# Performance work log

Hardware: AMD Instinct MI355X
Metric: run time of the kernel (lower is better)

Reference implementation:

```python
import jax, jax.numpy as jnp
import numpy as np

L, B, T, C, H, V = 4, 4, 1024, 1024, 16, 32000
DH = C // H
FF = 4 * C
IGNORE = 5
EPS = 1e-5


def setup_inputs() -> dict:
    key = jax.random.key(0)
    ks = jax.random.split(key, 12)
    s = 0.02
    return {
        "idx": jax.random.randint(ks[0], (B, T), 0, V),
        "targets": jax.random.randint(ks[1], (B, T), 0, V),
        "tok_emb": jax.random.normal(ks[2], (V, C), jnp.float32) * s,
        "pos_emb": jax.random.normal(ks[3], (T, C), jnp.float32) * s,
        "Wq": jax.random.normal(ks[4], (L, C, C), jnp.float32) * s,
        "Wk": jax.random.normal(ks[5], (L, C, C), jnp.float32) * s,
        "Wv": jax.random.normal(ks[6], (L, C, C), jnp.float32) * s,
        "Wo": jax.random.normal(ks[7], (L, C, C), jnp.float32) * s,
        "bo": jnp.zeros((L, C), jnp.float32),
        "ln1_g": jnp.ones((L, C), jnp.float32),
        "ln1_b": jnp.zeros((L, C), jnp.float32),
        "ln2_g": jnp.ones((L, C), jnp.float32),
        "ln2_b": jnp.zeros((L, C), jnp.float32),
        "W1": jax.random.normal(ks[8], (L, C, FF), jnp.float32) * s,
        "b1": jnp.zeros((L, FF), jnp.float32),
        "W2": jax.random.normal(ks[9], (L, FF, C), jnp.float32) * s,
        "b2": jnp.zeros((L, C), jnp.float32),
        "lnf_g": jnp.ones((C,), jnp.float32),
        "lnf_b": jnp.zeros((C,), jnp.float32),
        "Whead": jax.random.normal(ks[10], (C, V), jnp.float32) * s,
        "bhead": jnp.zeros((V,), jnp.float32),
    }


def _layernorm(x, g, b):
    mu = jnp.mean(x, axis=-1, keepdims=True)
    var = jnp.var(x, axis=-1, keepdims=True)
    return (x - mu) * jax.lax.rsqrt(var + EPS) * g + b


def _gpt_forward(idx, targets, tok_emb, pos_emb, Wq, Wk, Wv, Wo, bo,
                 ln1_g, ln1_b, ln2_g, ln2_b, W1, b1, W2, b2,
                 lnf_g, lnf_b, Whead, bhead):
    x = tok_emb[idx] + pos_emb[None, :, :]  # [B,T,C]
    causal = jnp.tril(jnp.ones((T, T), bool))
    for i in range(L):
        h = _layernorm(x, ln1_g[i], ln1_b[i])
        q = (h @ Wq[i]).reshape(B, T, H, DH)
        k = (h @ Wk[i]).reshape(B, T, H, DH)
        v = (h @ Wv[i]).reshape(B, T, H, DH)
        wei = jnp.einsum("bqhd,bkhd->bhqk", q, k) * (DH ** -0.5)
        wei = jnp.where(causal[None, None], wei, -jnp.inf)
        wei = jax.nn.softmax(wei, axis=-1)
        att = jnp.einsum("bhqk,bkhd->bqhd", wei, v).reshape(B, T, C)
        x = x + att @ Wo[i] + bo[i]
        h = _layernorm(x, ln2_g[i], ln2_b[i])
        x = x + jax.nn.gelu(h @ W1[i] + b1[i], approximate=False) @ W2[i] + b2[i]
    x = _layernorm(x, lnf_g, lnf_b)
    logits = x @ Whead + bhead  # [B,T,V]
    # cross-entropy with ignore_index=5
    lg = logits.reshape(B * T, V)
    tg = targets.reshape(B * T)
    logp = jax.nn.log_softmax(lg, axis=-1)
    nll = -jnp.take_along_axis(logp, tg[:, None], axis=-1)[:, 0]
    valid = (tg != IGNORE).astype(lg.dtype)
    loss = jnp.sum(nll * valid) / jnp.maximum(jnp.sum(valid), 1.0)
    return logits, loss


def reference(idx, targets, tok_emb, pos_emb, Wq, Wk, Wv, Wo, bo,
              ln1_g, ln1_b, ln2_g, ln2_b, W1, b1, W2, b2,
              lnf_g, lnf_b, Whead, bhead):
    return _gpt_forward(idx, targets, tok_emb, pos_emb, Wq, Wk, Wv, Wo, bo,
                        ln1_g, ln1_b, ln2_g, ln2_b, W1, b1, W2, b2,
                        lnf_g, lnf_b, Whead, bhead)
```

## Files before the change

kernel.cpp:

```cpp
#include <hip/hip_runtime.h>
#include <cstdint>
#include <cstddef>

#define Lx 4
#define Bx 4
#define Tx 1024
#define Cx 1024
#define Hx 16
#define DHx 64
#define FFx 4096
#define Vx 32000
#define BTx 4096

typedef __attribute__((ext_vector_type(8))) __bf16 bf16x8;
typedef __attribute__((ext_vector_type(4))) float f32x4;
typedef __attribute__((ext_vector_type(8))) short short8;

__device__ __forceinline__ float bflo(unsigned u){ return __builtin_bit_cast(float, u << 16); }
__device__ __forceinline__ float bf2f(short s){ return bflo((unsigned)(unsigned short)s); }
__device__ __forceinline__ short f2bf(float f){
  unsigned u = __builtin_bit_cast(unsigned, f);
  u += 0x7fffu + ((u >> 16) & 1u);
  return (short)(u >> 16);
}

__device__ __forceinline__ void gload_lds16(const short* g, short* l){
  __builtin_amdgcn_global_load_lds(
      (const __attribute__((address_space(1))) unsigned int*)g,
      (__attribute__((address_space(3))) unsigned int*)l, 16, 0, 0);
}

__device__ __forceinline__ int xcd_swizzle(int orig, int nwg){
  const int q = nwg >> 3, r = nwg & 7;
  const int xcd = orig & 7, wg = orig >> 3;
  const int base = (xcd < r) ? xcd * (q + 1) : r * (q + 1) + (xcd - r) * q;
  return base + wg;
}

__global__ __launch_bounds__(256) void embed_kernel(
    const int* __restrict__ idx, const float* __restrict__ tok,
    const float* __restrict__ pos, float* __restrict__ x)
{
  const int bt = blockIdx.x;
  const int t  = bt & (Tx - 1);
  const int tid = threadIdx.x;
  const int tk = idx[bt];
  float4 a = *(const float4*)&tok[((size_t)tk << 10) + (tid << 2)];
  const float4 p = *(const float4*)&pos[((size_t)t << 10) + (tid << 2)];
  a.x += p.x; a.y += p.y; a.z += p.z; a.w += p.w;
  *(float4*)&x[((size_t)bt << 10) + (tid << 2)] = a;
}

__global__ __launch_bounds__(256) void ln_kernel(
    const float* __restrict__ x, const float* __restrict__ g,
    const float* __restrict__ b, short* __restrict__ out)
{
  const int row = blockIdx.x;
  const int tid = threadIdx.x;
  const float4 v = *(const float4*)&x[((size_t)row << 10) + (tid << 2)];
  float s  = v.x + v.y + v.z + v.w;
  float ss = v.x*v.x + v.y*v.y + v.z*v.z + v.w*v.w;
  #pragma unroll
  for (int off = 32; off >= 1; off >>= 1) {
    s  += __shfl_down(s, off);
    ss += __shfl_down(ss, off);
  }
  __shared__ float rs[4], rss[4];
  const int lane = tid & 63, w = tid >> 6;
  if (lane == 0) { rs[w] = s; rss[w] = ss; }
  __syncthreads();
  s  = rs[0] + rs[1] + rs[2] + rs[3];
  ss = rss[0] + rss[1] + rss[2] + rss[3];
  const float mu  = s * (1.0f / Cx);
  const float var = ss * (1.0f / Cx) - mu * mu;
  const float rstd = rsqrtf(var + 1e-5f);
  const float4 g4 = *(const float4*)&g[tid << 2];
  const float4 b4 = *(const float4*)&b[tid << 2];
  short4 o;
  o.x = f2bf((v.x - mu) * rstd * g4.x + b4.x);
  o.y = f2bf((v.y - mu) * rstd * g4.y + b4.y);
  o.z = f2bf((v.z - mu) * rstd * g4.z + b4.z);
  o.w = f2bf((v.w - mu) * rstd * g4.w + b4.w);
  *(short4*)&out[((size_t)row << 10) + (tid << 2)] = o;
}

__global__ __launch_bounds__(256) void wconv_kernel(
    const float* __restrict__ W, short* __restrict__ Wt, int K, int N)
{
  __shared__ float tile[32][33];
  const int n0 = blockIdx.x << 5, k0 = blockIdx.y << 5;
  const int tx = threadIdx.x & 31, ty = threadIdx.x >> 5;
  #pragma unroll
  for (int r = 0; r < 4; ++r)
    tile[ty + (r << 3)][tx] = __builtin_nontemporal_load(
        &W[(size_t)(k0 + ty + (r << 3)) * N + n0 + tx]);
  __syncthreads();
  #pragma unroll
  for (int r = 0; r < 4; ++r)
    Wt[(size_t)(n0 + ty + (r << 3)) * K + k0 + tx] = f2bf(tile[tx][ty + (r << 3)]);
}

__global__ __launch_bounds__(256) void wconv4_kernel(
    const float* __restrict__ Wq, const float* __restrict__ Wk,
    const float* __restrict__ Wv, const float* __restrict__ Wo,
    short* __restrict__ qkvT, short* __restrict__ woT)
{
  __shared__ float tile[32][33];
  const int z = blockIdx.z;
  const float* W = (z == 0) ? Wq : (z == 1) ? Wk : (z == 2) ? Wv : Wo;
  short* Wt = (z < 3) ? qkvT + (size_t)z * Cx * Cx : woT;
  const int n0 = blockIdx.x << 5, k0 = blockIdx.y << 5;
  const int tx = threadIdx.x & 31, ty = threadIdx.x >> 5;
  #pragma unroll
  for (int r = 0; r < 4; ++r)
    tile[ty + (r << 3)][tx] = __builtin_nontemporal_load(
        &W[(size_t)(k0 + ty + (r << 3)) * Cx + n0 + tx]);
  __syncthreads();
  #pragma unroll
  for (int r = 0; r < 4; ++r)
    Wt[(size_t)(n0 + ty + (r << 3)) * Cx + k0 + tx] = f2bf(tile[tx][ty + (r << 3)]);
}

template<int MODE>
__global__ __launch_bounds__(256) void gemm_kernel(
    const short* __restrict__ A, const short* __restrict__ Bt,
    const float* __restrict__ bias, const float* __restrict__ res,
    float* __restrict__ outF, short* __restrict__ outB, int N, int K)
{
  __shared__ __align__(16) short sA[128 * 32];
  __shared__ __align__(16) short sB[128 * 32];
  const int tid  = threadIdx.x;
  const int lane = tid & 63;
  const int wave = tid >> 6;
  const int bid  = xcd_swizzle((int)blockIdx.x, (int)gridDim.x);
  const int tm = (bid & 31) << 7;
  const int tn = (bid >> 5) << 7;
  const int wm = ((wave >> 1) & 1) << 6;
  const int wn = (wave & 1) << 6;

  f32x4 acc[4][4] = {};

  const int o1  = tid << 4;
  const int row = o1 >> 6;
  const int col = (o1 & 63) >> 1;
  const short* gA1 = A  + (size_t)(tm + row) * K + col;
  const short* gA2 = A  + (size_t)(tm + row + 64) * K + col;
  const short* gB1 = Bt + (size_t)(tn + row) * K + col;
  const short* gB2 = Bt + (size_t)(tn + row + 64) * K + col;
  short* lA1 = sA + (wave << 9);
  short* lA2 = sA + 2048 + (wave << 9);
  short* lB1 = sB + (wave << 9);
  short* lB2 = sB + 2048 + (wave << 9);

  for (int k0 = 0; k0 < K; k0 += 32) {
    gload_lds16(gA1 + k0, lA1);
    gload_lds16(gA2 + k0, lA2);
    gload_lds16(gB1 + k0, lB1);
    gload_lds16(gB2 + k0, lB2);
    __syncthreads();
    bf16x8 aF[4], bF[4];
    const int kb = (lane >> 4) << 3;
    const int rsel = lane & 15;
    #pragma unroll
    for (int m = 0; m < 4; ++m)
      aF[m] = *(const bf16x8*)&sA[(wm + m * 16 + rsel) * 32 + kb];
    #pragma unroll
    for (int n = 0; n < 4; ++n)
      bF[n] = *(const bf16x8*)&sB[(wn + n * 16 + rsel) * 32 + kb];
    #pragma unroll
    for (int m = 0; m < 4; ++m) {
      #pragma unroll
      for (int n = 0; n < 4; ++n)
        acc[m][n] = __builtin_amdgcn_mfma_f32_16x16x32_bf16(aF[m], bF[n], acc[m][n], 0, 0, 0);
    }
    __syncthreads();
  }

  const int r0 = (lane >> 4) << 2;
  const int c0 = lane & 15;
  #pragma unroll
  for (int m = 0; m < 4; ++m) {
    #pragma unroll
    for (int n = 0; n < 4; ++n) {
      #pragma unroll
      for (int r = 0; r < 4; ++r) {
        const int grow = tm + wm + m * 16 + r0 + r;
        const int gcol = tn + wn + n * 16 + c0;
        const float v = acc[m][n][r];
        if constexpr (MODE == 0) {
          const int which = gcol >> 10;
          const int cc = gcol & 1023;
          const int b = grow >> 10, t = grow & 1023;
          const int hh = cc >> 6, d = cc & 63;
          outB[(size_t)which * (BTx * Cx) +
               ((size_t)((((b << 4) + hh) << 10) + t) << 6) + d] = f2bf(v);
        } else {
          const size_t o = (size_t)grow * N + gcol;
          outF[o] = res[o] + v + bias[gcol];
        }
      }
    }
  }
}

#define GBAR() do { __builtin_amdgcn_sched_barrier(0); __builtin_amdgcn_s_barrier(); __builtin_amdgcn_sched_barrier(0); } while(0)
#define VM4 asm volatile("s_waitcnt vmcnt(4)" ::: "memory");
#define VM0 asm volatile("s_waitcnt vmcnt(0)" ::: "memory");
#define NOWAIT

#define PHASE(qq, dd, STAGES, ENDW) do { \
  aF[0][0] = RD_A(dd, qq, 0, 0); aF[0][1] = RD_A(dd, qq, 0, 1); \
  aF[1][0] = RD_A(dd, qq, 1, 0); aF[1][1] = RD_A(dd, qq, 1, 1); \
  STAGES \
  GBAR(); \
  asm volatile("s_waitcnt lgkmcnt(0)" ::: "memory"); \
  __builtin_amdgcn_sched_barrier(0); \
  __builtin_amdgcn_s_setprio(1); \
  _Pragma("unroll") \
  for (int ks = 0; ks < 2; ++ks) { \
    _Pragma("unroll") \
    for (int mf = 0; mf < 2; ++mf) { \
      _Pragma("unroll") \
      for (int nf = 0; nf < 4; ++nf) \
        acc[((qq) << 1) + mf][nf] = __builtin_amdgcn_mfma_f32_16x16x32_bf16( \
            aF[mf][ks], bF[nf][ks], acc[((qq) << 1) + mf][nf], 0, 0, 0); \
    } \
  } \
  __builtin_amdgcn_s_setprio(0); \
  ENDW \
  GBAR(); \
} while (0)

#define BLOAD(dd) do { \
  _Pragma("unroll") \
  for (int nf = 0; nf < 4; ++nf) { bF[nf][0] = RD_B(dd, nf, 0); bF[nf][1] = RD_B(dd, nf, 1); } \
} while (0)

#define FINISH(qq) do { \
  _Pragma("unroll") \
  for (int m8 = ((qq) << 1); m8 < ((qq) << 1) + 2; ++m8) { \
    _Pragma("unroll") \
    for (int nf = 0; nf < 4; ++nf) { \
      _Pragma("unroll") \
      for (int r = 0; r < 4; ++r) { \
        const int grow = tm + (wm << 7) + (m8 << 4) + (g4 << 2) + r; \
        const int gcol = tn + (wn << 6) + (nf << 4) + r15; \
        if constexpr (MODE == 3) { \
          acc[m8][nf][r] += bb4[nf]; \
          outF[(size_t)grow * N + gcol] = acc[m8][nf][r]; \
        } else { \
          const float t2 = acc[m8][nf][r] + bb4[nf]; \
          const float gl = 0.5f * t2 * (1.0f + erff(t2 * 0.7071067811865475f)); \
          outB[(size_t)grow * N + gcol] = f2bf(gl); \
        } \
      } \
    } \
  } \
} while (0)

template<int MODE>
__global__ __launch_bounds__(512, 2) void gemm256_kernel(
    const short* __restrict__ A, const short* __restrict__ Bt,
    const float* __restrict__ bias, float* __restrict__ outF,
    short* __restrict__ outB, float* __restrict__ cep, int N, int K)
{
  __shared__ __align__(16) char lds[131072];
  const int tid  = threadIdx.x;
  const int lane = tid & 63;
  const int wid  = tid >> 6;
  const int wm   = wid >> 2;
  const int wn   = wid & 3;
  const int r15  = lane & 15;
  const int g4   = lane >> 4;
  const int bid  = xcd_swizzle((int)blockIdx.x, (int)gridDim.x);
  const int tm   = (bid & 15) << 8;
  const int tn   = (bid >> 4) << 8;
  const int NT   = K >> 6;
  const int NI   = NT >> 1;

  const int row0   = tid >> 3;
  const int innerE = ((tid & 7) ^ ((tid >> 3) & 7)) << 3;
  const int X0     = tid << 4;
  const short* srcA = A  + (size_t)(tm + row0) * K + innerE;
  const short* srcB = Bt + (size_t)(tn + row0) * K + innerE;
  const size_t h128K = (size_t)128 * K;
  const size_t r64K  = (size_t)64 * K;

  auto STAGE_A = [&](int t, int hh) {
    const short* s = srcA + (size_t)hh * h128K + (t << 6);
    char* d = lds + ((t & 1) << 15) + (hh << 14) + X0;
    gload_lds16(s, (short*)d);
    gload_lds16(s + r64K, (short*)(d + 8192));
  };
  auto STAGE_B = [&](int t, int hh) {
    const short* s = srcB + (size_t)hh * h128K + (t << 6);
    char* d = lds + 65536 + ((t & 1) << 15) + (hh << 14) + X0;
    gload_lds16(s, (short*)d);
    gload_lds16(s + r64K, (short*)(d + 8192));
  };

  const int arowb = (wm << 7) + r15;
  const int bcolb = (wn << 6) + r15;
  const int kchnk = g4 << 4;
  auto RD_A = [&](int d, int q, int mf, int ks) -> bf16x8 {
    const int row = arowb + (q << 5) + (mf << 4);
    return *(const bf16x8*)(lds + (d << 15) + (row << 7) +
                            ((((ks) << 6) + kchnk) ^ ((row & 7) << 4)));
  };
  auto RD_B = [&](int d, int nf, int ks) -> bf16x8 {
    const int colc = bcolb + (nf << 4);
    return *(const bf16x8*)(lds + 65536 + (d << 15) + (colc << 7) +
                            ((((ks) << 6) + kchnk) ^ ((colc & 7) << 4)));
  };

  f32x4 acc[8][4] = {};

  STAGE_A(0, 0); STAGE_A(0, 1); STAGE_B(0, 0); STAGE_B(0, 1);
  STAGE_B(1, 0); STAGE_B(1, 1);
  VM4
  GBAR();

  for (int i = 0; i < NI - 1; ++i) {
    const int t1 = 2 * i + 1;
    const int ta = 2 * i + 2;
    const int tb = 2 * i + 3;
    bf16x8 aF[2][2], bF[4][2];
    BLOAD(0);
    PHASE(0, 0, { STAGE_A(t1, 0); },                  NOWAIT);
    PHASE(1, 0, { STAGE_A(t1, 1); STAGE_B(ta, 0); },  NOWAIT);
    PHASE(2, 0, { STAGE_B(ta, 1); },                  NOWAIT);
    PHASE(3, 0, { },                                  VM4);
    BLOAD(1);
    PHASE(0, 1, { STAGE_A(ta, 0); },                  NOWAIT);
    PHASE(1, 1, { STAGE_A(ta, 1); STAGE_B(tb, 0); },  NOWAIT);
    PHASE(2, 1, { STAGE_B(tb, 1); },                  NOWAIT);
    PHASE(3, 1, { },                                  VM4);
  }

  float bb4[4];
  #pragma unroll
  for (int nf = 0; nf < 4; ++nf) bb4[nf] = bias[tn + (wn << 6) + (nf << 4) + r15];

  {
    bf16x8 aF[2][2], bF[4][2];
    BLOAD(0);
    PHASE(0, 0, { STAGE_A(NT - 1, 0); }, NOWAIT);
    PHASE(1, 0, { STAGE_A(NT - 1, 1); }, NOWAIT);
    PHASE(2, 0, { },                     NOWAIT);
    PHASE(3, 0, { },                     VM0);
    BLOAD(1);
    PHASE(0, 1, { }, NOWAIT); FINISH(0);
    PHASE(1, 1, { }, NOWAIT); FINISH(1);
    PHASE(2, 1, { }, NOWAIT); FINISH(2);
    PHASE(3, 1, { }, NOWAIT); FINISH(3);
  }

  if constexpr (MODE == 3) {
    const int nb = tn >> 8;
    float* cepart = (float*)lds;
    #pragma unroll
    for (int m8 = 0; m8 < 8; ++m8) {
      #pragma unroll
      for (int r = 0; r < 4; ++r) {
        float sm = __expf(acc[m8][0][r]) + __expf(acc[m8][1][r])
                 + __expf(acc[m8][2][r]) + __expf(acc[m8][3][r]);
        sm += __shfl_xor(sm, 1);
        sm += __shfl_xor(sm, 2);
        sm += __shfl_xor(sm, 4);
        sm += __shfl_xor(sm, 8);
        if (r15 == 0)
          cepart[(wn << 8) + (wm << 7) + (m8 << 4) + (g4 << 2) + r] = sm;
      }
    }
    __syncthreads();
    if (tid < 256) {
      const float S = cepart[tid] + cepart[256 + tid] + cepart[512 + tid] + cepart[768 + tid];
      cep[(size_t)(tm + tid) * 125 + nb] = S;
    }
  }
}

__global__ __launch_bounds__(256) void fattn_kernel(
    const short* __restrict__ q, const short* __restrict__ k,
    const short* __restrict__ v, short* __restrict__ att)
{
  __shared__ __align__(16) short sQ[4096];
  __shared__ __align__(16) short sK[2][4096];
  __shared__ __align__(16) short sVT[2][4096];
  __shared__ __align__(16) short sP[4][1024];

  const int tid  = threadIdx.x;
  const int lane = tid & 63;
  const int w    = tid >> 6;
  const int r15  = lane & 15;
  const int g4   = lane >> 4;
  const int bid  = xcd_swizzle((int)blockIdx.x, (int)gridDim.x);
  const int qt   = bid & 15;
  const int bh   = bid >> 4;

  const char* Qb = (const char*)(q + ((size_t)bh << 16)) + ((size_t)qt << 13);
  const char* Kb = (const char*)(k + ((size_t)bh << 16));
  const char* Vb = (const char*)(v + ((size_t)bh << 16));

  const int X0  = tid << 4;
  const int X1  = X0 + 4096;
  const int sw0 = X0 ^ (((X0 >> 7) & 7) << 4);
  const int sw1 = X1 ^ (((X1 >> 7) & 7) << 4);
  const int ldsOff0 = (w << 10);
  const int ldsOff1 = (w << 10) + 4096;

  const int vdh  = (lane & 31) << 1;
  const int vkv0 = (((w << 1) + (lane >> 5)) << 3);
  const int vb0  = (vdh * 128 + vkv0 * 2)       ^ ((vdh & 7) << 4);
  const int vb1  = ((vdh + 1) * 128 + vkv0 * 2) ^ (((vdh + 1) & 7) << 4);

  auto loadV = [&](int kt, unsigned* uv) {
    const char* Vt = Vb + ((size_t)kt << 13);
    #pragma unroll
    for (int j = 0; j < 8; ++j)
      uv[j] = *(const unsigned*)(Vt + ((vkv0 + j) << 7) + (vdh << 1));
  };
  auto writeV = [&](int buf, const unsigned* uv) {
    short8 plo, phi;
    #pragma unroll
    for (int j = 0; j < 8; ++j) {
      plo[j] = (short)(uv[j] & 0xffffu);
      phi[j] = (short)(uv[j] >> 16);
    }
    *(short8*)((char*)sVT[buf] + vb0) = plo;
    *(short8*)((char*)sVT[buf] + vb1) = phi;
  };
  auto stageK = [&](int kt, int buf) {
    const char* Kt = Kb + ((size_t)kt << 13);
    gload_lds16((const short*)(Kt + sw0), (short*)((char*)sK[buf] + ldsOff0));
    gload_lds16((const short*)(Kt + sw1), (short*)((char*)sK[buf] + ldsOff1));
  };

  gload_lds16((const short*)(Qb + sw0), (short*)((char*)sQ + ldsOff0));
  gload_lds16((const short*)(Qb + sw1), (short*)((char*)sQ + ldsOff1));
  stageK(0, 0);
  {
    unsigned uv[8];
    loadV(0, uv);
    writeV(0, uv);
  }
  __syncthreads();

  bf16x8 aQ[2];
  {
    const int qrow = (w << 4) + r15;
    const int base = qrow * 128 + (g4 << 4);
    const int sz = (qrow & 7) << 4;
    aQ[0] = *(const bf16x8*)((char*)sQ + ((base     ) ^ sz));
    aQ[1] = *(const bf16x8*)((char*)sQ + ((base + 64) ^ sz));
  }

  float m[4] = {-3e38f, -3e38f, -3e38f, -3e38f};
  float l[4] = {0.f, 0.f, 0.f, 0.f};
  f32x4 acc_o[4] = {};
  const int qrow_g0 = (qt << 6) + (w << 4) + (g4 << 2);

  for (int kt = 0; kt <= qt; ++kt) {
    const int cur = kt & 1;
    unsigned uv2[8];
    if (kt < qt) {
      stageK(kt + 1, cur ^ 1);
      loadV(kt + 1, uv2);
    }

    f32x4 s[4] = {};
    #pragma unroll
    for (int f = 0; f < 4; ++f) {
      const int kv = (f << 4) + r15;
      const int kb = kv * 128 + (g4 << 4);
      const int sz = (kv & 7) << 4;
      const bf16x8 b0 = *(const bf16x8*)((char*)sK[cur] + ((kb     ) ^ sz));
      const bf16x8 b1 = *(const bf16x8*)((char*)sK[cur] + ((kb + 64) ^ sz));
      s[f] = __builtin_amdgcn_mfma_f32_16x16x32_bf16(aQ[0], b0, s[f], 0, 0, 0);
      s[f] = __builtin_amdgcn_mfma_f32_16x16x32_bf16(aQ[1], b1, s[f], 0, 0, 0);
    }
    #pragma unroll
    for (int f = 0; f < 4; ++f) {
      #pragma unroll
      for (int r = 0; r < 4; ++r) {
        float sv = s[f][r] * 0.125f;
        if ((kt << 6) + (f << 4) + r15 > qrow_g0 + r) sv = -3e38f;
        s[f][r] = sv;
      }
    }
    #pragma unroll
    for (int r = 0; r < 4; ++r) {
      float mx = fmaxf(fmaxf(s[0][r], s[1][r]), fmaxf(s[2][r], s[3][r]));
      mx = fmaxf(mx, __shfl_xor(mx, 1));
      mx = fmaxf(mx, __shfl_xor(mx, 2));
      mx = fmaxf(mx, __shfl_xor(mx, 4));
      mx = fmaxf(mx, __shfl_xor(mx, 8));
      const float mn = fmaxf(m[r], mx);
      const float e  = __expf(m[r] - mn);
      float sum = 0.f;
      #pragma unroll
      for (int f = 0; f < 4; ++f) {
        const float p = __expf(s[f][r] - mn);
        s[f][r] = p; sum += p;
      }
      sum += __shfl_xor(sum, 1);
      sum += __shfl_xor(sum, 2);
      sum += __shfl_xor(sum, 4);
      sum += __shfl_xor(sum, 8);
      l[r] = l[r] * e + sum;
      m[r] = mn;
      acc_o[0][r] *= e; acc_o[1][r] *= e; acc_o[2][r] *= e; acc_o[3][r] *= e;
    }
    short* Pw = sP[w];
    #pragma unroll
    for (int f = 0; f < 4; ++f) {
      #pragma unroll
      for (int r = 0; r < 4; ++r) {
        const int prow = (g4 << 2) + r;
        const int byte = prow * 128 + (((f << 4) + r15) << 1);
        *(short*)((char*)Pw + (byte ^ ((prow & 7) << 4))) = f2bf(s[f][r]);
      }
    }
    #pragma unroll
    for (int ks = 0; ks < 2; ++ks) {
      const int ab = r15 * 128 + (ks << 6) + (g4 << 4);
      const bf16x8 aP = *(const bf16x8*)((char*)Pw + (ab ^ ((r15 & 7) << 4)));
      #pragma unroll
      for (int f = 0; f < 4; ++f) {
        const int dh = (f << 4) + r15;
        const int bb = dh * 128 + (ks << 6) + (g4 << 4);
        const bf16x8 bV = *(const bf16x8*)((char*)sVT[cur] + (bb ^ ((dh & 7) << 4)));
        acc_o[f] = __builtin_amdgcn_mfma_f32_16x16x32_bf16(aP, bV, acc_o[f], 0, 0, 0);
      }
    }

    if (kt < qt) writeV(cur ^ 1, uv2);
    __syncthreads();
  }

  const int b = bh >> 4, hh = bh & 15;
  #pragma unroll
  for (int f = 0; f < 4; ++f) {
    #pragma unroll
    for (int r = 0; r < 4; ++r) {
      const int qg = qrow_g0 + r;
      const int dh = (f << 4) + r15;
      att[((size_t)((b << 10) + qg) << 10) + (hh << 6) + dh] = f2bf(acc_o[f][r] / l[r]);
    }
  }
}

__global__ __launch_bounds__(256) void ce_lse_kernel(
    const float* __restrict__ part, const float* __restrict__ logits,
    const int* __restrict__ tgt, float2* __restrict__ nll)
{
  const int row  = blockIdx.x * 4 + (threadIdx.x >> 6);
  const int lane = threadIdx.x & 63;
  float S = 0.f;
  #pragma unroll
  for (int p = 0; p < 2; ++p) {
    const int i = lane + (p << 6);
    if (i < 125) S += part[(size_t)row * 125 + i];
  }
  #pragma unroll
  for (int off = 32; off >= 1; off >>= 1) S += __shfl_xor(S, off);
  if (lane == 0) {
    const int tg = tgt[row];
    float v = 0.f, cnt = 0.f;
    if (tg != 5) {
      const float lt = logits[(size_t)row * Vx + tg];
      v = -(lt - logf(S));
      cnt = 1.f;
    }
    float2 o2; o2.x = v; o2.y = cnt;
    nll[row] = o2;
  }
}

__global__ __launch_bounds__(256) void ce_sum_kernel(
    const float2* __restrict__ nll, float* __restrict__ out)
{
  const int tid = threadIdx.x;
  float s = 0.f, c = 0.f;
  #pragma unroll
  for (int i = 0; i < 16; ++i) {
    const float2 v = nll[tid * 16 + i];
    s += v.x; c += v.y;
  }
  __shared__ float ls[256], lc[256];
  ls[tid] = s; lc[tid] = c;
  __syncthreads();
  for (int off = 128; off >= 1; off >>= 1) {
    if (tid < off) { ls[tid] += ls[tid + off]; lc[tid] += lc[tid + off]; }
    __syncthreads();
  }
  if (tid == 0) out[131072000ull] = ls[0] / fmaxf(lc[0], 1.0f);
}

extern "C" void kernel_launch(void* const* d_in, const int* in_sizes, int n_in,
                              void* d_out, int out_size, void* d_ws, size_t ws_size,
                              hipStream_t stream)
{
  const int*   idx     = (const int*)d_in[0];
  const int*   targets = (const int*)d_in[1];
  const float* tok_emb = (const float*)d_in[2];
  const float* pos_emb = (const float*)d_in[3];
  const float* Wq      = (const float*)d_in[4];
  const float* Wk      = (const float*)d_in[5];
  const float* Wv      = (const float*)d_in[6];
  const float* Wo      = (const float*)d_in[7];
  const float* bo      = (const float*)d_in[8];
  const float* ln1_g   = (const float*)d_in[9];
  const float* ln1_b   = (const float*)d_in[10];
  const float* ln2_g   = (const float*)d_in[11];
  const float* ln2_b   = (const float*)d_in[12];
  const float* W1      = (const float*)d_in[13];
  const float* b1      = (const float*)d_in[14];
  const float* W2      = (const float*)d_in[15];
  const float* b2      = (const float*)d_in[16];
  const float* lnf_g   = (const float*)d_in[17];
  const float* lnf_b   = (const float*)d_in[18];
  const float* Whead   = (const float*)d_in[19];
  const float* bhead   = (const float*)d_in[20];
  float* out = (float*)d_out;

  char* ws = (char*)d_ws;
  size_t off = 0;
  auto alloc = [&](size_t bytes) -> char* {
    char* p = ws + off;
    off += (bytes + 255) & ~(size_t)255;
    return p;
  };
  float* x    = (float*)alloc((size_t)BTx * Cx * 4);
  short* h    = (short*)alloc((size_t)BTx * Cx * 2);
  char*  blk  = ws + off;
  short* qb   = (short*)alloc((size_t)BTx * Cx * 2);
  short* kb   = (short*)alloc((size_t)BTx * Cx * 2);
  short* vb   = (short*)alloc((size_t)BTx * Cx * 2);
  short* attb = (short*)alloc((size_t)BTx * Cx * 2);
  short* ffb  = (short*)alloc((size_t)BTx * FFx * 2);
  short* wheadT = (short*)blk;
  short* wqkvT = (short*)alloc((size_t)3 * Cx * Cx * 2);
  short* woT  = (short*)alloc((size_t)Cx * Cx * 2);
  short* w1T  = (short*)alloc((size_t)Cx * FFx * 2);
  short* w2T  = (short*)alloc((size_t)FFx * Cx * 2);
  if (ws_size < off) return;
  float* part  = (float*)wqkvT;
  float2* nllb = (float2*)woT;

  embed_kernel<<<BTx, 256, 0, stream>>>(idx, tok_emb, pos_emb, x);

  for (int i = 0; i < Lx; ++i) {
    const size_t wo_off = (size_t)i * Cx * Cx;
    const size_t w1_off = (size_t)i * Cx * FFx;
    wconv4_kernel<<<dim3(Cx / 32, Cx / 32, 4), 256, 0, stream>>>(
        Wq + wo_off, Wk + wo_off, Wv + wo_off, Wo + wo_off, wqkvT, woT);
    wconv_kernel<<<dim3(FFx / 32, Cx / 32), 256, 0, stream>>>(W1 + w1_off, w1T, Cx, FFx);
    wconv_kernel<<<dim3(Cx / 32, FFx / 32), 256, 0, stream>>>(W2 + w1_off, w2T, FFx, Cx);

    ln_kernel<<<BTx, 256, 0, stream>>>(x, ln1_g + i * Cx, ln1_b + i * Cx, h);
    gemm_kernel<0><<<32 * 24, 256, 0, stream>>>(h, wqkvT, nullptr, nullptr, nullptr, qb, 3 * Cx, Cx);
    fattn_kernel<<<Bx * Hx * (Tx / 64), 256, 0, stream>>>(qb, kb, vb, attb);
    gemm_kernel<1><<<32 * 8, 256, 0, stream>>>(attb, woT, bo + i * Cx, x, x, nullptr, Cx, Cx);

    ln_kernel<<<BTx, 256, 0, stream>>>(x, ln2_g + i * Cx, ln2_b + i * Cx, h);
    gemm256_kernel<2><<<16 * 16, 512, 0, stream>>>(h, w1T, b1 + i * FFx, nullptr, ffb, nullptr, FFx, Cx);
    gemm_kernel<1><<<32 * 8, 256, 0, stream>>>(ffb, w2T, b2 + i * Cx, x, x, nullptr, Cx, FFx);
  }

  ln_kernel<<<BTx, 256, 0, stream>>>(x, lnf_g, lnf_b, h);
  wconv_kernel<<<dim3(Vx / 32, Cx / 32), 256, 0, stream>>>(Whead, wheadT, Cx, Vx);
  gemm256_kernel<3><<<16 * 125, 512, 0, stream>>>(h, wheadT, bhead, out, nullptr, part, Vx, Cx);

  ce_lse_kernel<<<BTx / 4, 256, 0, stream>>>(part, out, targets, nllb);
  ce_sum_kernel<<<1, 256, 0, stream>>>(nllb, out);
}
```

Before: 1.554 ms.

## Use wave-per-row layernorm, merge per-layer weight conversions, prioritize attention MFMA

The layernorm kernel now handles one row per wave, four rows per block, and reduces with xor shuffles, so the shared-memory reduction and block barrier are gone. The three per-layer weight transpose/convert launches are merged into one kernel with a flat block index that selects the QKV/O, W1 or W2 tile. The flash-attention kernel raises wave priority around its MFMA sections with s_setprio. Together these aim to cut launch count and synchronisation overhead, at the cost of more branching in the merged conversion kernel.

```diff
diff --git a/kernel.cpp b/kernel.cpp
--- a/kernel.cpp
+++ b/kernel.cpp
@@ -55,33 +55,38 @@
     const float* __restrict__ x, const float* __restrict__ g,
     const float* __restrict__ b, short* __restrict__ out)
 {
-  const int row = blockIdx.x;
-  const int tid = threadIdx.x;
-  const float4 v = *(const float4*)&x[((size_t)row << 10) + (tid << 2)];
-  float s  = v.x + v.y + v.z + v.w;
-  float ss = v.x*v.x + v.y*v.y + v.z*v.z + v.w*v.w;
+  const int row  = (blockIdx.x << 2) + (threadIdx.x >> 6);
+  const int lane = threadIdx.x & 63;
+  const float* xr = x + ((size_t)row << 10);
+  float4 v[4];
+  float s = 0.f, ss = 0.f;
+  #pragma unroll
+  for (int j = 0; j < 4; ++j) {
+    v[j] = *(const float4*)&xr[(lane << 2) + (j << 8)];
+    s  += v[j].x + v[j].y + v[j].z + v[j].w;
+    ss += v[j].x*v[j].x + v[j].y*v[j].y + v[j].z*v[j].z + v[j].w*v[j].w;
+  }
   #pragma unroll
   for (int off = 32; off >= 1; off >>= 1) {
-    s  += __shfl_down(s, off);
-    ss += __shfl_down(ss, off);
-  }
-  __shared__ float rs[4], rss[4];
-  const int lane = tid & 63, w = tid >> 6;
-  if (lane == 0) { rs[w] = s; rss[w] = ss; }
-  __syncthreads();
-  s  = rs[0] + rs[1] + rs[2] + rs[3];
-  ss = rss[0] + rss[1] + rss[2] + rss[3];
+    s  += __shfl_xor(s, off);
+    ss += __shfl_xor(ss, off);
+  }
   const float mu  = s * (1.0f / Cx);
   const float var = ss * (1.0f / Cx) - mu * mu;
   const float rstd = rsqrtf(var + 1e-5f);
-  const float4 g4 = *(const float4*)&g[tid << 2];
-  const float4 b4 = *(const float4*)&b[tid << 2];
-  short4 o;
-  o.x = f2bf((v.x - mu) * rstd * g4.x + b4.x);
-  o.y = f2bf((v.y - mu) * rstd * g4.y + b4.y);
-  o.z = f2bf((v.z - mu) * rstd * g4.z + b4.z);
-  o.w = f2bf((v.w - mu) * rstd * g4.w + b4.w);
-  *(short4*)&out[((size_t)row << 10) + (tid << 2)] = o;
+  short* or_ = out + ((size_t)row << 10);
+  #pragma unroll
+  for (int j = 0; j < 4; ++j) {
+    const int c = (lane << 2) + (j << 8);
+    const float4 g4 = *(const float4*)&g[c];
+    const float4 b4 = *(const float4*)&b[c];
+    short4 o;
+    o.x = f2bf((v[j].x - mu) * rstd * g4.x + b4.x);
+    o.y = f2bf((v[j].y - mu) * rstd * g4.y + b4.y);
+    o.z = f2bf((v[j].z - mu) * rstd * g4.z + b4.z);
+    o.w = f2bf((v[j].w - mu) * rstd * g4.w + b4.w);
+    *(short4*)&or_[c] = o;
+  }
 }
 
 __global__ __launch_bounds__(256) void wconv_kernel(
@@ -100,25 +105,40 @@
     Wt[(size_t)(n0 + ty + (r << 3)) * K + k0 + tx] = f2bf(tile[tx][ty + (r << 3)]);
 }
 
-__global__ __launch_bounds__(256) void wconv4_kernel(
+__global__ __launch_bounds__(256) void wconvL_kernel(
     const float* __restrict__ Wq, const float* __restrict__ Wk,
     const float* __restrict__ Wv, const float* __restrict__ Wo,
-    short* __restrict__ qkvT, short* __restrict__ woT)
+    const float* __restrict__ W1, const float* __restrict__ W2,
+    short* __restrict__ qkvT, short* __restrict__ woT,
+    short* __restrict__ w1T, short* __restrict__ w2T)
 {
   __shared__ float tile[32][33];
-  const int z = blockIdx.z;
-  const float* W = (z == 0) ? Wq : (z == 1) ? Wk : (z == 2) ? Wv : Wo;
-  short* Wt = (z < 3) ? qkvT + (size_t)z * Cx * Cx : woT;
-  const int n0 = blockIdx.x << 5, k0 = blockIdx.y << 5;
+  const int id = blockIdx.x;
+  const float* W; short* Wt; int K, N, n0, k0;
+  if (id < 4096) {
+    const int z = id >> 10, t = id & 1023;
+    W  = (z == 0) ? Wq : (z == 1) ? Wk : (z == 2) ? Wv : Wo;
+    Wt = (z < 3) ? qkvT + (size_t)z * Cx * Cx : woT;
+    K = Cx; N = Cx;
+    n0 = (t & 31) << 5; k0 = (t >> 5) << 5;
+  } else if (id < 8192) {
+    const int t = id - 4096;
+    W = W1; Wt = w1T; K = Cx; N = FFx;
+    n0 = (t & 127) << 5; k0 = (t >> 7) << 5;
+  } else {
+    const int t = id - 8192;
+    W = W2; Wt = w2T; K = FFx; N = Cx;
+    n0 = (t & 31) << 5; k0 = (t >> 5) << 5;
+  }
   const int tx = threadIdx.x & 31, ty = threadIdx.x >> 5;
   #pragma unroll
   for (int r = 0; r < 4; ++r)
     tile[ty + (r << 3)][tx] = __builtin_nontemporal_load(
-        &W[(size_t)(k0 + ty + (r << 3)) * Cx + n0 + tx]);
+        &W[(size_t)(k0 + ty + (r << 3)) * N + n0 + tx]);
   __syncthreads();
   #pragma unroll
   for (int r = 0; r < 4; ++r)
-    Wt[(size_t)(n0 + ty + (r << 3)) * Cx + k0 + tx] = f2bf(tile[tx][ty + (r << 3)]);
+    Wt[(size_t)(n0 + ty + (r << 3)) * K + k0 + tx] = f2bf(tile[tx][ty + (r << 3)]);
 }
 
 template<int MODE>
@@ -469,6 +489,7 @@
     }
 
     f32x4 s[4] = {};
+    __builtin_amdgcn_s_setprio(1);
     #pragma unroll
     for (int f = 0; f < 4; ++f) {
       const int kv = (f << 4) + r15;
@@ -479,6 +500,7 @@
       s[f] = __builtin_amdgcn_mfma_f32_16x16x32_bf16(aQ[0], b0, s[f], 0, 0, 0);
       s[f] = __builtin_amdgcn_mfma_f32_16x16x32_bf16(aQ[1], b1, s[f], 0, 0, 0);
     }
+    __builtin_amdgcn_s_setprio(0);
     #pragma unroll
     for (int f = 0; f < 4; ++f) {
       #pragma unroll
@@ -521,6 +543,7 @@
         *(short*)((char*)Pw + (byte ^ ((prow & 7) << 4))) = f2bf(s[f][r]);
       }
     }
+    __builtin_amdgcn_s_setprio(1);
     #pragma unroll
     for (int ks = 0; ks < 2; ++ks) {
       const int ab = r15 * 128 + (ks << 6) + (g4 << 4);
@@ -533,6 +556,7 @@
         acc_o[f] = __builtin_amdgcn_mfma_f32_16x16x32_bf16(aP, bV, acc_o[f], 0, 0, 0);
       }
     }
+    __builtin_amdgcn_s_setprio(0);
 
     if (kt < qt) writeV(cur ^ 1, uv2);
     __syncthreads();
@@ -653,22 +677,21 @@
   for (int i = 0; i < Lx; ++i) {
     const size_t wo_off = (size_t)i * Cx * Cx;
     const size_t w1_off = (size_t)i * Cx * FFx;
-    wconv4_kernel<<<dim3(Cx / 32, Cx / 32, 4), 256, 0, stream>>>(
-        Wq + wo_off, Wk + wo_off, Wv + wo_off, Wo + wo_off, wqkvT, woT);
-    wconv_kernel<<<dim3(FFx / 32, Cx / 32), 256, 0, stream>>>(W1 + w1_off, w1T, Cx, FFx);
-    wconv_kernel<<<dim3(Cx / 32, FFx / 32), 256, 0, stream>>>(W2 + w1_off, w2T, FFx, Cx);
-
-    ln_kernel<<<BTx, 256, 0, stream>>>(x, ln1_g + i * Cx, ln1_b + i * Cx, h);
+    wconvL_kernel<<<12288, 256, 0, stream>>>(
+        Wq + wo_off, Wk + wo_off, Wv + wo_off, Wo + wo_off,
+        W1 + w1_off, W2 + w1_off, wqkvT, woT, w1T, w2T);
+
+    ln_kernel<<<BTx / 4, 256, 0, stream>>>(x, ln1_g + i * Cx, ln1_b + i * Cx, h);
     gemm_kernel<0><<<32 * 24, 256, 0, stream>>>(h, wqkvT, nullptr, nullptr, nullptr, qb, 3 * Cx, Cx);
     fattn_kernel<<<Bx * Hx * (Tx / 64), 256, 0, stream>>>(qb, kb, vb, attb);
     gemm_kernel<1><<<32 * 8, 256, 0, stream>>>(attb, woT, bo + i * Cx, x, x, nullptr, Cx, Cx);
 
-    ln_kernel<<<BTx, 256, 0, stream>>>(x, ln2_g + i * Cx, ln2_b + i * Cx, h);
+    ln_kernel<<<BTx / 4, 256, 0, stream>>>(x, ln2_g + i * Cx, ln2_b + i * Cx, h);
     gemm256_kernel<2><<<16 * 16, 512, 0, stream>>>(h, w1T, b1 + i * FFx, nullptr, ffb, nullptr, FFx, Cx);
     gemm_kernel<1><<<32 * 8, 256, 0, stream>>>(ffb, w2T, b2 + i * Cx, x, x, nullptr, Cx, FFx);
   }
 
-  ln_kernel<<<BTx, 256, 0, stream>>>(x, lnf_g, lnf_b, h);
+  ln_kernel<<<BTx / 4, 256, 0, stream>>>(x, lnf_g, lnf_b, h);
   wconv_kernel<<<dim3(Vx / 32, Cx / 32), 256, 0, stream>>>(Whead, wheadT, Cx, Vx);
   gemm256_kernel<3><<<16 * 125, 512, 0, stream>>>(h, wheadT, bhead, out, nullptr, part, Vx, Cx);
 
```

Result: no change. 1.549 ms (-0.4%).
